# Kernel optimization log

Hardware: AMD Instinct MI355X
Metric: run time of the kernel (lower is better)

## Reference

```python
import jax, jax.numpy as jnp
import numpy as np

B, H, S, Dh = 4, 16, 2048, 64
NEG = -1.0e9


def setup_inputs() -> dict:
    key = jax.random.key(0)
    kq, kk, kv = jax.random.split(key, 3)
    q = jax.random.normal(kq, (B, H, S, Dh), dtype=jnp.float32)
    k = jax.random.normal(kk, (B, H, S, Dh), dtype=jnp.float32)
    v = jax.random.normal(kv, (B, H, S, Dh), dtype=jnp.float32)
    # causal mask: 1.0 where attention is disallowed (j > i), matching mask * -1e9
    mask = jnp.triu(jnp.ones((S, S), dtype=jnp.float32), k=1)[None, None, :, :]
    return {"q": q, "k": k, "v": v, "mask": mask}


def reference(q, k, v, mask):
    # scaled dot-product attention: softmax(QK^T / sqrt(Dh) + mask * -1e9) V
    dim_k = jnp.asarray(k.shape[-1], dtype=jnp.float32)
    logits = jnp.einsum("bhsd,bhtd->bhst", q, k) / jnp.sqrt(dim_k)
    logits = logits + mask * NEG
    weights = jax.nn.softmax(logits, axis=-1)
    return jnp.einsum("bhst,bhtd->bhsd", weights, v)
```

## Files before the change

### kernel.cpp

```cpp
#include <hip/hip_runtime.h>

#define S_LEN 2048
#define DH 64

typedef float f32x4 __attribute__((ext_vector_type(4)));
typedef __bf16 bf16x8 __attribute__((ext_vector_type(8)));

#define PTS 72
#define MFMA16(A, B, C) __builtin_amdgcn_mfma_f32_16x16x32_bf16(A, B, C, 0, 0, 0)

__device__ __forceinline__ unsigned short f2bf(float f) {
    unsigned u = __builtin_bit_cast(unsigned, f);
    u += 0x7fffu + ((u >> 16) & 1u);
    return (unsigned short)(u >> 16);
}

__device__ __forceinline__ uint4 pack8(const float* s) {
    unsigned short h[8];
#pragma unroll
    for (int i = 0; i < 8; ++i) h[i] = f2bf(s[i]);
    return *(const uint4*)h;
}

__device__ __forceinline__ unsigned pack_tr(float a, float b) {
    return __builtin_amdgcn_perm(__builtin_bit_cast(unsigned, b),
                                 __builtin_bit_cast(unsigned, a), 0x07060302u);
}

__device__ __forceinline__ bf16x8 ld128(const unsigned short* p) {
    return __builtin_bit_cast(bf16x8, *(const uint4*)p);
}

__device__ __forceinline__ bf16x8 ones8() {
    uint4 ou; ou.x = 0x3F803F80u; ou.y = ou.x; ou.z = ou.x; ou.w = ou.x;
    return __builtin_bit_cast(bf16x8, ou);
}

__global__ __launch_bounds__(256) void prep_kv(const float* __restrict__ k,
                                               const float* __restrict__ v,
                                               uint4* __restrict__ kimg,
                                               uint4* __restrict__ vimg) {
    __shared__ unsigned short tr[64 * 40];
    const int bid = blockIdx.x;
    const int t = threadIdx.x;
    if (bid < 4096) {
        const int r = t >> 3, b = t & 7;
        const int srcblk = b ^ (r & 7);
        const float* src = k + ((size_t)bid * 32 + r) * 64 + srcblk * 8;
        float buf[8];
        *(float4*)&buf[0] = *(const float4*)src;
        *(float4*)&buf[4] = *(const float4*)(src + 4);
        kimg[(size_t)bid * 256 + t] = pack8(buf);
    } else {
        const int vb = bid - 4096;
        const int r = t >> 3, cb = t & 7;
        const float* src = v + ((size_t)vb * 32 + r) * 64 + cb * 8;
        float buf[8];
        *(float4*)&buf[0] = *(const float4*)src;
        *(float4*)&buf[4] = *(const float4*)(src + 4);
#pragma unroll
        for (int i = 0; i < 8; ++i)
            tr[(cb * 8 + i) * 40 + r] = f2bf(buf[i]);
        __syncthreads();
        const int d = t >> 2, kb = t & 3;
        const int skb = kb ^ ((d >> 1) & 3);
        vimg[(size_t)vb * 256 + t] = *(const uint4*)&tr[d * 40 + skb * 8];
    }
}

template <int DIAG>
__device__ __forceinline__ void body64(
    const unsigned short* __restrict__ kt, const unsigned short* __restrict__ vt,
    unsigned short* __restrict__ pw0, unsigned short* __restrict__ pw1,
    const bf16x8* qf, f32x4 acc[2][4], f32x4* accl,
    int jt, int qbase, int quad, int c)
{
    const int sw = c & 7;
    const bf16x8 ones = ones8();
    const int MTN = (DIAG == 1) ? 2 : 4;

#pragma unroll
    for (int mt = 0; mt < MTN; ++mt) {
        const unsigned short* kr = kt + (mt * 16 + c) * 64;
        bf16x8 ka0 = ld128(kr + ((quad ^ sw) << 3));
        bf16x8 ka1 = ld128(kr + (((quad | 4) ^ sw) << 3));
        f32x4 s0 = (f32x4){0.f, 0.f, 0.f, 0.f};
        f32x4 s1 = (f32x4){0.f, 0.f, 0.f, 0.f};
        s0 = MFMA16(ka0, qf[0], s0);  s0 = MFMA16(ka1, qf[1], s0);
        s1 = MFMA16(ka0, qf[2], s1);  s1 = MFMA16(ka1, qf[3], s1);

        const bool MASKMT = (DIAG == 1) || (DIAG == 2 && mt >= 2);
#pragma unroll
        for (int s = 0; s < 2; ++s) {
            const f32x4 st = s ? s1 : s0;
            const int ig = qbase + s * 16 + c;
            float p[4];
#pragma unroll
            for (int r = 0; r < 4; ++r) {
                float e = __builtin_amdgcn_exp2f(st[r]);
                if (MASKMT) {
                    const int jg = jt * 64 + mt * 16 + quad * 4 + r;
                    e = (jg > ig) ? 0.f : e;
                }
                p[r] = e;
            }
            unsigned a = pack_tr(p[0], p[1]);
            unsigned b = pack_tr(p[2], p[3]);
            unsigned* pb = (unsigned*)(s ? pw1 : pw0) + c * (PTS / 2) + mt * 8 + quad * 2;
            *(uint2*)pb = make_uint2(a, b);
        }
    }

    bf16x8 pf00 = ld128(pw0 + c * PTS + quad * 8);
    bf16x8 pf10 = ld128(pw1 + c * PTS + quad * 8);
    accl[0] = MFMA16(pf00, ones, accl[0]);
    accl[1] = MFMA16(pf10, ones, accl[1]);
    bf16x8 pf01, pf11;
    if (DIAG != 1) {
        pf01 = ld128(pw0 + c * PTS + 32 + quad * 8);
        pf11 = ld128(pw1 + c * PTS + 32 + quad * 8);
        accl[0] = MFMA16(pf01, ones, accl[0]);
        accl[1] = MFMA16(pf11, ones, accl[1]);
    }

    const int vsw = (c >> 1) & 3;
#pragma unroll
    for (int dc = 0; dc < 4; ++dc) {
        const unsigned short* vr = vt + (dc * 16 + c) * 32 + ((quad ^ vsw) << 3);
        bf16x8 vf0 = ld128(vr);
        acc[0][dc] = MFMA16(pf00, vf0, acc[0][dc]);
        acc[1][dc] = MFMA16(pf10, vf0, acc[1][dc]);
        if (DIAG != 1) {
            bf16x8 vf1 = ld128(vr + 2048);
            acc[0][dc] = MFMA16(pf01, vf1, acc[0][dc]);
            acc[1][dc] = MFMA16(pf11, vf1, acc[1][dc]);
        }
    }
}

__global__ __launch_bounds__(256, 4) void fa_kernel(
    const float* __restrict__ q,
    const uint4* __restrict__ kimg,
    const uint4* __restrict__ vimg,
    float* __restrict__ out)
{
    __shared__ unsigned short kt[64 * 64];
    __shared__ unsigned short vt[2 * 64 * 32];
    __shared__ unsigned short pt[4][2][16 * PTS];

    const int tid  = threadIdx.x;
    const int lane = tid & 63;
    const int wave = tid >> 6;
    const int quad = lane >> 4;
    const int c    = lane & 15;

    const int bid = blockIdx.x;
    const int bh  = bid & 63;
    static const int qperm[16] = {15, 14, 13, 12, 8, 9, 10, 11,
                                  6, 5, 4, 3, 1, 2, 7, 0};
    const int qblk = qperm[bid >> 6];

    const int wt      = qblk * 4 + wave;
    const int qbase   = wt * 32;
    const int my_diag = wt >> 1;
    const int jt_last = 2 * qblk + 1;

    const size_t head_off = (size_t)bh * S_LEN * DH;

    const float SCALE = 0.125f * 1.4426950408889634f;
    bf16x8 qf[4];
#pragma unroll
    for (int s = 0; s < 2; ++s) {
        const float* qrow = q + head_off + (size_t)(qbase + s * 16 + c) * DH;
        float t0[8], t1[8];
#pragma unroll
        for (int i = 0; i < 8; ++i) t0[i] = qrow[quad * 8 + i] * SCALE;
#pragma unroll
        for (int i = 0; i < 8; ++i) t1[i] = qrow[32 + quad * 8 + i] * SCALE;
        qf[s * 2 + 0] = __builtin_bit_cast(bf16x8, pack8(t0));
        qf[s * 2 + 1] = __builtin_bit_cast(bf16x8, pack8(t1));
    }

    f32x4 acc[2][4];
#pragma unroll
    for (int s = 0; s < 2; ++s)
#pragma unroll
        for (int dc = 0; dc < 4; ++dc) acc[s][dc] = (f32x4){0.f, 0.f, 0.f, 0.f};
    f32x4 accl[2];
    accl[0] = (f32x4){0.f, 0.f, 0.f, 0.f};
    accl[1] = (f32x4){0.f, 0.f, 0.f, 0.f};

    const uint4* kin = kimg + (size_t)bh * 64 * 256 + tid;
    const uint4* vin = vimg + (size_t)bh * 64 * 256 + tid;
    unsigned short* pw0 = pt[wave][0];
    unsigned short* pw1 = pt[wave][1];

    uint4 kA = kin[0], kB = kin[256];
    uint4 vA = vin[0], vB = vin[256];
    for (int jt = 0; jt <= jt_last; ++jt) {
        __syncthreads();
        ((uint4*)kt)[tid] = kA;  ((uint4*)kt)[tid + 256] = kB;
        ((uint4*)vt)[tid] = vA;  ((uint4*)vt)[tid + 256] = vB;
        if (jt < jt_last) {
            kA = kin[(jt + 1) * 512];  kB = kin[(jt + 1) * 512 + 256];
            vA = vin[(jt + 1) * 512];  vB = vin[(jt + 1) * 512 + 256];
        }
        __syncthreads();

        if (jt < my_diag) {
            body64<0>(kt, vt, pw0, pw1, qf, acc, accl, jt, qbase, quad, c);
        } else if (jt == my_diag) {
            if ((wt & 1) == 0)
                body64<1>(kt, vt, pw0, pw1, qf, acc, accl, jt, qbase, quad, c);
            else
                body64<2>(kt, vt, pw0, pw1, qf, acc, accl, jt, qbase, quad, c);
        }
    }

    float* ob = out + head_off;
#pragma unroll
    for (int s = 0; s < 2; ++s) {
        float linv[4];
#pragma unroll
        for (int r = 0; r < 4; ++r) linv[r] = 1.0f / accl[s][r];
#pragma unroll
        for (int dc = 0; dc < 4; ++dc)
#pragma unroll
            for (int r = 0; r < 4; ++r) {
                const size_t idx =
                    (size_t)(qbase + s * 16 + quad * 4 + r) * DH + dc * 16 + c;
                ob[idx] = acc[s][dc][r] * linv[r];
            }
    }
}

#define KT_STRIDE 88
#define VT_STRIDE 36
__global__ __launch_bounds__(256) void fa_kernel_fb(
    const float* __restrict__ q, const float* __restrict__ k,
    const float* __restrict__ v, float* __restrict__ out)
{
    __shared__ unsigned short kts[32 * KT_STRIDE];
    __shared__ unsigned short vts[64 * VT_STRIDE];
    __shared__ unsigned short pts[4][16 * 40];
    const int tid = threadIdx.x, lane = tid & 63, wave = tid >> 6;
    const int quad = lane >> 4, c = lane & 15;
    const int bid = blockIdx.x, bh = bid & 63, qblk = 31 - (bid >> 6);
    const int qtile = qblk * 4 + wave, qbase = qtile * 16;
    const int my_diag = qtile >> 1, jt_last = (qblk * 4 + 3) >> 1;
    const size_t head_off = (size_t)bh * S_LEN * DH;
    const float* qrow = q + head_off + (size_t)(qbase + c) * DH;
    float qtmp[8];
#pragma unroll
    for (int i = 0; i < 8; ++i) qtmp[i] = qrow[quad * 8 + i];
    bf16x8 qf0 = __builtin_bit_cast(bf16x8, pack8(qtmp));
#pragma unroll
    for (int i = 0; i < 8; ++i) qtmp[i] = qrow[32 + quad * 8 + i];
    bf16x8 qf1 = __builtin_bit_cast(bf16x8, pack8(qtmp));
    f32x4 acc[4];
#pragma unroll
    for (int dc = 0; dc < 4; ++dc) acc[dc] = (f32x4){0.f, 0.f, 0.f, 0.f};
    float m_run = -1e30f, l_run = 0.f;
    const int ig = qbase + c;
    const int srow = tid >> 3, sdb = tid & 7;
    const int vcol = (((srow >> 3) ^ (sdb & 3)) << 3) | (srow & 7);
    const float LOG2E = 1.4426950408889634f;
    for (int jt = 0; jt <= jt_last; ++jt) {
        __syncthreads();
        {
            const size_t g = head_off + (size_t)(jt * 32 + srow) * DH + sdb * 8;
            float kbuf[8];
            *(float4*)&kbuf[0] = *(const float4*)(k + g);
            *(float4*)&kbuf[4] = *(const float4*)(k + g + 4);
            *(uint4*)&kts[srow * KT_STRIDE + sdb * 8] = pack8(kbuf);
            float vbuf[8];
            *(float4*)&vbuf[0] = *(const float4*)(v + g);
            *(float4*)&vbuf[4] = *(const float4*)(v + g + 4);
#pragma unroll
            for (int i = 0; i < 8; ++i)
                vts[(sdb * 8 + i) * VT_STRIDE + vcol] = f2bf(vbuf[i]);
        }
        __syncthreads();
        if (jt > my_diag) continue;
        f32x4 st[2];
#pragma unroll
        for (int mt = 0; mt < 2; ++mt) {
            const unsigned short* krow = &kts[(mt * 16 + c) * KT_STRIDE + quad * 8];
            bf16x8 ka0 = __builtin_bit_cast(bf16x8, *(const uint4*)krow);
            bf16x8 ka1 = __builtin_bit_cast(bf16x8, *(const uint4*)(krow + 32));
            f32x4 a = (f32x4){0.f, 0.f, 0.f, 0.f};
            a = MFMA16(ka0, qf0, a);
            a = MFMA16(ka1, qf1, a);
            st[mt] = a;
        }
        float tv[8];
#pragma unroll
        for (int mt = 0; mt < 2; ++mt)
#pragma unroll
            for (int r = 0; r < 4; ++r) {
                const int jg = jt * 32 + mt * 16 + quad * 4 + r;
                const float s = st[mt][r] * 0.125f;
                tv[mt * 4 + r] = (jg > ig) ? -1e30f : s;
            }
        float tm = tv[0];
#pragma unroll
        for (int i = 1; i < 8; ++i) tm = fmaxf(tm, tv[i]);
        tm = fmaxf(tm, __shfl_xor(tm, 16, 64));
        tm = fmaxf(tm, __shfl_xor(tm, 32, 64));
        const float m_new = fmaxf(m_run, tm);
        const float mb = m_new * LOG2E;
        float p[8], ps = 0.f;
#pragma unroll
        for (int i = 0; i < 8; ++i) {
            p[i] = __builtin_amdgcn_exp2f(tv[i] * LOG2E - mb);
            ps += p[i];
        }
        ps += __shfl_xor(ps, 16, 64);
        ps += __shfl_xor(ps, 32, 64);
        const float alpha = __builtin_amdgcn_exp2f((m_run - m_new) * LOG2E);
        l_run = l_run * alpha + ps;
        m_run = m_new;
        unsigned short* pwf = pts[wave];
#pragma unroll
        for (int mt = 0; mt < 2; ++mt)
#pragma unroll
            for (int r = 0; r < 4; ++r)
                pwf[c * 40 + mt * 16 + quad * 4 + r] = f2bf(p[mt * 4 + r]);
        float ar[4];
#pragma unroll
        for (int r = 0; r < 4; ++r)
            ar[r] = __shfl(alpha, (quad << 4) + quad * 4 + r, 64);
#pragma unroll
        for (int dc = 0; dc < 4; ++dc)
#pragma unroll
            for (int r = 0; r < 4; ++r) acc[dc][r] *= ar[r];
        bf16x8 pf = __builtin_bit_cast(bf16x8, *(const uint4*)&pwf[c * 40 + quad * 8]);
#pragma unroll
        for (int dc = 0; dc < 4; ++dc) {
            const int vrow = dc * 16 + c;
            const int blk = quad ^ ((vrow >> 3) & 3);
            const unsigned short* vp = &vts[vrow * VT_STRIDE + blk * 8];
            uint2 a0 = *(const uint2*)vp;
            uint2 a1 = *(const uint2*)(vp + 4);
            uint4 u; u.x = a0.x; u.y = a0.y; u.z = a1.x; u.w = a1.y;
            bf16x8 vf = __builtin_bit_cast(bf16x8, u);
            acc[dc] = MFMA16(pf, vf, acc[dc]);
        }
    }
    float linv[4];
#pragma unroll
    for (int r = 0; r < 4; ++r) {
        const float lr = __shfl(l_run, (quad << 4) + quad * 4 + r, 64);
        linv[r] = 1.0f / lr;
    }
    float* ob = out + head_off;
#pragma unroll
    for (int dc = 0; dc < 4; ++dc)
#pragma unroll
        for (int r = 0; r < 4; ++r) {
            const size_t idx = (size_t)(qbase + quad * 4 + r) * DH + dc * 16 + c;
            ob[idx] = acc[dc][r] * linv[r];
        }
}

extern "C" void kernel_launch(void* const* d_in, const int* in_sizes, int n_in,
                              void* d_out, int out_size, void* d_ws, size_t ws_size,
                              hipStream_t stream) {
    const float* q = (const float*)d_in[0];
    const float* k = (const float*)d_in[1];
    const float* v = (const float*)d_in[2];
    float* o = (float*)d_out;
    const size_t need = (size_t)2 * 64 * 64 * 4096;
    if (ws_size >= need) {
        uint4* kimg = (uint4*)d_ws;
        uint4* vimg = kimg + (size_t)64 * 64 * 256;
        hipLaunchKernelGGL(prep_kv, dim3(8192), dim3(256), 0, stream, k, v, kimg, vimg);
        hipLaunchKernelGGL(fa_kernel, dim3(1024), dim3(256), 0, stream, q, kimg, vimg, o);
    } else {
        hipLaunchKernelGGL(fa_kernel_fb, dim3(2048), dim3(256), 0, stream, q, k, v, o);
    }
}
```

Baseline: 186.2 us.

## Pair mirrored 16-row query tiles per wave to balance causal work

Each wave now handles two 16-row query tiles, one from block pi and one from the mirrored block 31-pi, instead of 32 contiguous rows. Every workgroup therefore does the same amount of causal work, and the qperm ordering table is no longer needed. The loop body is templated on per-tile mask modes, and masked diagonal sub-tiles are skipped with zero-fill. The aim is to remove load imbalance across workgroups, at the cost of more branching inside the per-tile loop and each tile using only half of the loaded K/V on some iterations.

```diff
diff --git a/kernel.cpp b/kernel.cpp
--- a/kernel.cpp
+++ b/kernel.cpp
@@ -68,72 +68,85 @@
     }
 }
 
-template <int DIAG>
+template <int SM>
+__device__ __forceinline__ void sub_mt(
+    const bf16x8 ka0, const bf16x8 ka1, const bf16x8 q0, const bf16x8 q1,
+    unsigned short* __restrict__ pw, int mt, int wave, int quad, int c)
+{
+    unsigned* pb = (unsigned*)pw + c * (PTS / 2) + mt * 8 + quad * 2;
+    if (SM == 2 && mt > wave) {
+        *(uint2*)pb = make_uint2(0u, 0u);
+        return;
+    }
+    f32x4 s = (f32x4){0.f, 0.f, 0.f, 0.f};
+    s = MFMA16(ka0, q0, s);
+    s = MFMA16(ka1, q1, s);
+    float p[4];
+#pragma unroll
+    for (int r = 0; r < 4; ++r) {
+        float e = __builtin_amdgcn_exp2f(s[r]);
+        if (SM == 2 && mt == wave) e = (quad * 4 + r > c) ? 0.f : e;
+        p[r] = e;
+    }
+    *(uint2*)pb = make_uint2(pack_tr(p[0], p[1]), pack_tr(p[2], p[3]));
+}
+
+template <int AM, int BM>
 __device__ __forceinline__ void body64(
     const unsigned short* __restrict__ kt, const unsigned short* __restrict__ vt,
     unsigned short* __restrict__ pw0, unsigned short* __restrict__ pw1,
     const bf16x8* qf, f32x4 acc[2][4], f32x4* accl,
-    int jt, int qbase, int quad, int c)
+    int wave, int quad, int c)
 {
     const int sw = c & 7;
     const bf16x8 ones = ones8();
-    const int MTN = (DIAG == 1) ? 2 : 4;
-
-#pragma unroll
-    for (int mt = 0; mt < MTN; ++mt) {
-        const unsigned short* kr = kt + (mt * 16 + c) * 64;
-        bf16x8 ka0 = ld128(kr + ((quad ^ sw) << 3));
-        bf16x8 ka1 = ld128(kr + (((quad | 4) ^ sw) << 3));
-        f32x4 s0 = (f32x4){0.f, 0.f, 0.f, 0.f};
-        f32x4 s1 = (f32x4){0.f, 0.f, 0.f, 0.f};
-        s0 = MFMA16(ka0, qf[0], s0);  s0 = MFMA16(ka1, qf[1], s0);
-        s1 = MFMA16(ka0, qf[2], s1);  s1 = MFMA16(ka1, qf[3], s1);
-
-        const bool MASKMT = (DIAG == 1) || (DIAG == 2 && mt >= 2);
-#pragma unroll
-        for (int s = 0; s < 2; ++s) {
-            const f32x4 st = s ? s1 : s0;
-            const int ig = qbase + s * 16 + c;
-            float p[4];
-#pragma unroll
-            for (int r = 0; r < 4; ++r) {
-                float e = __builtin_amdgcn_exp2f(st[r]);
-                if (MASKMT) {
-                    const int jg = jt * 64 + mt * 16 + quad * 4 + r;
-                    e = (jg > ig) ? 0.f : e;
-                }
-                p[r] = e;
-            }
-            unsigned a = pack_tr(p[0], p[1]);
-            unsigned b = pack_tr(p[2], p[3]);
-            unsigned* pb = (unsigned*)(s ? pw1 : pw0) + c * (PTS / 2) + mt * 8 + quad * 2;
-            *(uint2*)pb = make_uint2(a, b);
-        }
-    }
-
-    bf16x8 pf00 = ld128(pw0 + c * PTS + quad * 8);
-    bf16x8 pf10 = ld128(pw1 + c * PTS + quad * 8);
-    accl[0] = MFMA16(pf00, ones, accl[0]);
-    accl[1] = MFMA16(pf10, ones, accl[1]);
-    bf16x8 pf01, pf11;
-    if (DIAG != 1) {
-        pf01 = ld128(pw0 + c * PTS + 32 + quad * 8);
-        pf11 = ld128(pw1 + c * PTS + 32 + quad * 8);
-        accl[0] = MFMA16(pf01, ones, accl[0]);
-        accl[1] = MFMA16(pf11, ones, accl[1]);
+
+#pragma unroll
+    for (int mt = 0; mt < 4; ++mt) {
+        bf16x8 ka0 = ones, ka1 = ones;
+        const bool need_k = (AM == 1 || BM == 1) || (mt <= wave);
+        if (need_k) {
+            const unsigned short* kr = kt + (mt * 16 + c) * 64;
+            ka0 = ld128(kr + ((quad ^ sw) << 3));
+            ka1 = ld128(kr + (((quad | 4) ^ sw) << 3));
+        }
+        if constexpr (AM != 0) sub_mt<AM>(ka0, ka1, qf[0], qf[1], pw0, mt, wave, quad, c);
+        if constexpr (BM != 0) sub_mt<BM>(ka0, ka1, qf[2], qf[3], pw1, mt, wave, quad, c);
+    }
+
+    const bool hA = (AM == 1) || (wave >= 2);
+    const bool hB = (BM == 1) || (wave >= 2);
+
+    bf16x8 pfA0 = ones, pfA1 = ones, pfB0 = ones, pfB1 = ones;
+    if constexpr (AM != 0) {
+        pfA0 = ld128(pw0 + c * PTS + quad * 8);
+        accl[0] = MFMA16(pfA0, ones, accl[0]);
+        if (hA) {
+            pfA1 = ld128(pw0 + c * PTS + 32 + quad * 8);
+            accl[0] = MFMA16(pfA1, ones, accl[0]);
+        }
+    }
+    if constexpr (BM != 0) {
+        pfB0 = ld128(pw1 + c * PTS + quad * 8);
+        accl[1] = MFMA16(pfB0, ones, accl[1]);
+        if (hB) {
+            pfB1 = ld128(pw1 + c * PTS + 32 + quad * 8);
+            accl[1] = MFMA16(pfB1, ones, accl[1]);
+        }
     }
 
     const int vsw = (c >> 1) & 3;
 #pragma unroll
     for (int dc = 0; dc < 4; ++dc) {
         const unsigned short* vr = vt + (dc * 16 + c) * 32 + ((quad ^ vsw) << 3);
-        bf16x8 vf0 = ld128(vr);
-        acc[0][dc] = MFMA16(pf00, vf0, acc[0][dc]);
-        acc[1][dc] = MFMA16(pf10, vf0, acc[1][dc]);
-        if (DIAG != 1) {
-            bf16x8 vf1 = ld128(vr + 2048);
-            acc[0][dc] = MFMA16(pf01, vf1, acc[0][dc]);
-            acc[1][dc] = MFMA16(pf11, vf1, acc[1][dc]);
+        const bf16x8 vf0 = ld128(vr);
+        if constexpr (AM != 0) acc[0][dc] = MFMA16(pfA0, vf0, acc[0][dc]);
+        if constexpr (BM != 0) acc[1][dc] = MFMA16(pfB0, vf0, acc[1][dc]);
+        const bool need2 = (AM != 0 && hA) || (BM != 0 && hB);
+        if (need2) {
+            const bf16x8 vf1 = ld128(vr + 2048);
+            if constexpr (AM != 0) { if (hA) acc[0][dc] = MFMA16(pfA1, vf1, acc[0][dc]); }
+            if constexpr (BM != 0) { if (hB) acc[1][dc] = MFMA16(pfB1, vf1, acc[1][dc]); }
         }
     }
 }
@@ -156,14 +169,11 @@
 
     const int bid = blockIdx.x;
     const int bh  = bid & 63;
-    static const int qperm[16] = {15, 14, 13, 12, 8, 9, 10, 11,
-                                  6, 5, 4, 3, 1, 2, 7, 0};
-    const int qblk = qperm[bid >> 6];
-
-    const int wt      = qblk * 4 + wave;
-    const int qbase   = wt * 32;
-    const int my_diag = wt >> 1;
-    const int jt_last = 2 * qblk + 1;
+    const int pi  = bid >> 6;
+
+    const int qa = (pi * 4 + wave) * 16;
+    const int qb = ((31 - pi) * 4 + wave) * 16;
+    const int jt_last = 31 - pi;
 
     const size_t head_off = (size_t)bh * S_LEN * DH;
 
@@ -171,7 +181,8 @@
     bf16x8 qf[4];
 #pragma unroll
     for (int s = 0; s < 2; ++s) {
-        const float* qrow = q + head_off + (size_t)(qbase + s * 16 + c) * DH;
+        const int base = s ? qb : qa;
+        const float* qrow = q + head_off + (size_t)(base + c) * DH;
         float t0[8], t1[8];
 #pragma unroll
         for (int i = 0; i < 8; ++i) t0[i] = qrow[quad * 8 + i] * SCALE;
@@ -207,19 +218,20 @@
         }
         __syncthreads();
 
-        if (jt < my_diag) {
-            body64<0>(kt, vt, pw0, pw1, qf, acc, accl, jt, qbase, quad, c);
-        } else if (jt == my_diag) {
-            if ((wt & 1) == 0)
-                body64<1>(kt, vt, pw0, pw1, qf, acc, accl, jt, qbase, quad, c);
-            else
-                body64<2>(kt, vt, pw0, pw1, qf, acc, accl, jt, qbase, quad, c);
-        }
+        if (jt < pi)
+            body64<1, 1>(kt, vt, pw0, pw1, qf, acc, accl, wave, quad, c);
+        else if (jt == pi)
+            body64<2, 1>(kt, vt, pw0, pw1, qf, acc, accl, wave, quad, c);
+        else if (jt < jt_last)
+            body64<0, 1>(kt, vt, pw0, pw1, qf, acc, accl, wave, quad, c);
+        else
+            body64<0, 2>(kt, vt, pw0, pw1, qf, acc, accl, wave, quad, c);
     }
 
     float* ob = out + head_off;
 #pragma unroll
     for (int s = 0; s < 2; ++s) {
+        const int base = s ? qb : qa;
         float linv[4];
 #pragma unroll
         for (int r = 0; r < 4; ++r) linv[r] = 1.0f / accl[s][r];
@@ -228,7 +240,7 @@
 #pragma unroll
             for (int r = 0; r < 4; ++r) {
                 const size_t idx =
-                    (size_t)(qbase + s * 16 + quad * 4 + r) * DH + dc * 16 + c;
+                    (size_t)(base + quad * 4 + r) * DH + dc * 16 + c;
                 ob[idx] = acc[s][dc][r] * linv[r];
             }
     }
```

Measured after the change: 236.3 us. +26.9%, slower.
